# Kernel tuning notes

Hardware: AMD Instinct MI355X
Metric: run time of the kernel (lower is better)

## Reference

```python
import jax, jax.numpy as jnp
import numpy as np

B, T, W, D = 4, 1000, 32, 200
ED, N, DCONV, DTR = 400, 16, 4, 13  # d_inner=2*d_model, d_state, d_conv, dt_rank=ceil(200/16)


def _causal_conv(x, w, b):
    # x: (B, L, ED), depthwise causal conv, kernel DCONV
    L = x.shape[1]
    xp = jnp.pad(x, ((0, 0), (DCONV - 1, 0), (0, 0)))
    y = sum(xp[:, k:k + L, :] * w[:, k] for k in range(DCONV))
    return y + b


def _ssm(x, A_log, Dp, xproj, dtw, dtb):
    # selective scan; x: (B, L, ED)
    A = -jnp.exp(A_log)                      # (ED, N)
    dbc = x @ xproj                          # (B, L, DTR+2N)
    delta, Bm, Cm = dbc[..., :DTR], dbc[..., DTR:DTR + N], dbc[..., DTR + N:]
    dt = jax.nn.softplus(delta @ dtw + dtb)  # (B, L, ED)
    dA = jnp.exp(dt[..., None] * A)                         # (B, L, ED, N)
    dBx = dt[..., None] * Bm[:, :, None, :] * x[..., None]  # (B, L, ED, N)

    def step(h, t):
        dA_t, dBx_t, C_t = t
        h = dA_t * h + dBx_t
        y = jnp.einsum('ben,bn->be', h, C_t)
        return h, y

    h0 = jnp.zeros((x.shape[0], ED, N), x.dtype)
    xs = (dA.transpose(1, 0, 2, 3), dBx.transpose(1, 0, 2, 3), Cm.transpose(1, 0, 2))
    _, ys = jax.lax.scan(step, h0, xs)
    return ys.transpose(1, 0, 2) + Dp * x


def _branch(x, in_proj, conv_w, conv_b, xproj, dtw, dtb, A_log, Dp):
    xz = x @ in_proj
    xp, z = xz[..., :ED], xz[..., ED:]
    xp = jax.nn.silu(_causal_conv(xp, conv_w, conv_b))
    y = _ssm(xp, A_log, Dp, xproj, dtw, dtb)
    return y * jax.nn.silu(z)


def setup_inputs() -> dict:
    key = jax.random.key(0)
    ks = jax.random.split(key, 24)
    s = 0.02
    nrm = lambda k, shape: jax.random.normal(k, shape, jnp.float32) * s
    inp = {}
    inp['input_ids'] = jax.random.normal(ks[0], (B, T, W, D), jnp.float32)
    inp['n_tweets'] = jax.random.randint(ks[1], (B,), 1, T + 1)
    inp['n_words'] = jax.random.randint(ks[2], (B, T), 1, W + 1)
    inp['cls_token'] = jnp.zeros((1, 1, D), jnp.float32)
    inp['w_attn'] = nrm(ks[3], (D, 1))
    inp['b_attn'] = jnp.zeros((1,), jnp.float32)
    inp['norm_w'] = jnp.ones((D,), jnp.float32)
    for i, d in enumerate(('f', 'b')):
        o = i * 8
        inp[f'in_proj_{d}'] = nrm(ks[4 + o], (D, 2 * ED))
        inp[f'conv_w_{d}'] = nrm(ks[5 + o], (ED, DCONV))
        inp[f'conv_b_{d}'] = jnp.zeros((ED,), jnp.float32)
        inp[f'xproj_{d}'] = nrm(ks[6 + o], (ED, DTR + 2 * N))
        inp[f'dtw_{d}'] = nrm(ks[7 + o], (DTR, ED))
        inp[f'dtb_{d}'] = jnp.zeros((ED,), jnp.float32)
        inp[f'A_log_{d}'] = jnp.log(jnp.broadcast_to(jnp.arange(1, N + 1, dtype=jnp.float32), (ED, N)))
        inp[f'D_{d}'] = jnp.ones((ED,), jnp.float32)
    inp['out_proj'] = nrm(ks[20], (ED, D))
    inp['head_w'] = nrm(ks[21], (D, 1))
    inp['head_b'] = jnp.zeros((1,), jnp.float32)
    return inp


def reference(input_ids, n_tweets, n_words, cls_token, w_attn, b_attn, norm_w,
              in_proj_f, conv_w_f, conv_b_f, xproj_f, dtw_f, dtb_f, A_log_f, D_f,
              in_proj_b, conv_w_b, conv_b_b, xproj_b, dtw_b, dtb_b, A_log_b, D_b,
              out_proj, head_w, head_b):
    Bz, Tz, Wz, Dz = input_ids.shape
    # ragged per-tweet attention pooling, fully vectorized with masks
    scores = jnp.squeeze(input_ids @ w_attn, -1) + b_attn[0]        # (B, T, W)
    wmask = jnp.arange(Wz) < n_words[..., None]                     # (B, T, W)
    scores = jnp.where(wmask, scores, -jnp.inf)
    attn = jax.nn.softmax(scores, axis=-1)
    tw = jnp.einsum('btw,btwd->btd', attn, input_ids)               # (B, T, D)
    tmask = jnp.arange(Tz) < n_tweets[:, None]
    tw = jnp.where(tmask[..., None], tw, 0.0)                       # padded tweets stay zero
    pos = Tz // 2
    x = jnp.concatenate([tw[:, :pos], jnp.broadcast_to(cls_token, (Bz, 1, Dz)), tw[:, pos:]], axis=1)
    # one bidirectional Mamba layer: pre-RMSNorm residual block
    xn = x * jax.lax.rsqrt(jnp.mean(x * x, axis=-1, keepdims=True) + 1e-5) * norm_w
    y_f = _branch(xn, in_proj_f, conv_w_f, conv_b_f, xproj_f, dtw_f, dtb_f, A_log_f, D_f)
    y_b = jnp.flip(_branch(jnp.flip(xn, 1), in_proj_b, conv_w_b, conv_b_b, xproj_b, dtw_b, dtb_b, A_log_b, D_b), 1)
    x = x + (y_f + y_b) @ out_proj
    logit = jnp.squeeze(x[:, pos] @ head_w, -1) + head_b[0]
    return jax.nn.sigmoid(logit)
```

## Files before the change

kernel.cpp:

```cpp
#include <hip/hip_runtime.h>
#include <cmath>

#define Bz 4
#define Tz 1000
#define Wz 32
#define Dz 200
#define EDz 400
#define Nz 16
#define DTRz 13
#define Lz 1001
#define POSz 500
#define LPz 501
#define TSTR 512
#define ESP 10
#define NEG_BIG -1e30f

__device__ __forceinline__ float wave_sum(float v) {
#pragma unroll
  for (int o = 32; o; o >>= 1) v += __shfl_xor(v, o);
  return v;
}

__global__ __launch_bounds__(256) void k_front(
    const float* __restrict__ x, const int* __restrict__ n_tweets,
    const int* __restrict__ n_words, const float* __restrict__ w_attn,
    const float* __restrict__ b_attn, const float* __restrict__ norm_w,
    const float* __restrict__ cls, const float* __restrict__ out_proj,
    const float* __restrict__ head_w, const float* __restrict__ ipf,
    const float* __restrict__ ipb, float* __restrict__ xn,
    float* __restrict__ zbuf, float* __restrict__ vbuf) {
  int bid = blockIdx.x;
  int tid = threadIdx.x;
  if (bid < 9) {
    if (bid == 0) {
      __shared__ float hw[Dz];
      if (tid < Dz) hw[tid] = head_w[tid];
      __syncthreads();
      for (int e = tid; e < EDz; e += 256) {
        float acc = 0.f;
        for (int d = 0; d < Dz; d += 4) {
          float4 ov = *(const float4*)(out_proj + e * Dz + d);
          acc += ov.x * hw[d] + ov.y * hw[d + 1] + ov.z * hw[d + 2] + ov.w * hw[d + 3];
        }
        vbuf[e] = acc;
      }
      return;
    }
    int id = bid - 1;
    int br = id >> 2, b = id & 3;
    __shared__ float xs[Dz];
    __shared__ float s_red[4];
    float val = (tid < Dz) ? cls[tid] : 0.f;
    float sq = wave_sum(val * val);
    if ((tid & 63) == 0) s_red[tid >> 6] = sq;
    __syncthreads();
    float tot = s_red[0] + s_red[1] + s_red[2] + s_red[3];
    float scale = rsqrtf(tot * (1.f / Dz) + 1e-5f);
    if (tid < Dz) {
      float o = val * scale * norm_w[tid];
      xs[tid] = o;
      if (br == 0) xn[((size_t)b * Lz + POSz) * Dz + tid] = o;
    }
    __syncthreads();
    const float* ip = br ? ipb : ipf;
    for (int e = tid; e < EDz; e += 256) {
      float acc = 0.f;
      for (int d = 0; d < Dz; ++d) acc += xs[d] * ip[d * (2 * EDz) + EDz + e];
      zbuf[((size_t)br * Bz + b) * EDz + e] = acc;
    }
    return;
  }
  int blk = bid - 9;
  int b = blk / Tz, t = blk - b * Tz;
  int l = (t < POSz) ? t : t + 1;
  float* outp = xn + ((size_t)b * Lz + l) * Dz;
  int ntw = n_tweets[b]; if (ntw > Tz) ntw = Tz;
  if (t >= ntw) { if (tid < Dz) outp[tid] = 0.f; return; }
  int nw = n_words[b * Tz + t]; if (nw > Wz) nw = Wz; if (nw < 1) nw = 1;
  const float* xs = x + ((size_t)(b * Tz + t)) * (Wz * Dz);
  __shared__ float s_attn[Wz];
  __shared__ float s_red[4];
  int w = tid >> 3, j = tid & 7;
  float sc = 0.f;
  if (w < nw) {
    for (int d = j * 4; d < Dz; d += 32) {
      float4 xv = *(const float4*)(xs + w * Dz + d);
      float4 wv = *(const float4*)(w_attn + d);
      sc += xv.x * wv.x + xv.y * wv.y + xv.z * wv.z + xv.w * wv.w;
    }
  }
  sc += __shfl_xor(sc, 1); sc += __shfl_xor(sc, 2); sc += __shfl_xor(sc, 4);
  if (j == 0) s_attn[w] = (w < nw) ? (sc + b_attn[0]) : NEG_BIG;
  __syncthreads();
  if (tid < 64) {
    float s = (tid < Wz) ? s_attn[tid] : NEG_BIG;
    float m = s;
#pragma unroll
    for (int o = 32; o; o >>= 1) m = fmaxf(m, __shfl_xor(m, o));
    float e = (s > 0.5f * NEG_BIG) ? __expf(s - m) : 0.f;
    float tot = wave_sum(e);
    if (tid < Wz) s_attn[tid] = e / tot;
  }
  __syncthreads();
  float val = 0.f;
  if (tid < Dz) {
    for (int ww = 0; ww < nw; ++ww) val += s_attn[ww] * xs[ww * Dz + tid];
  }
  float sq = wave_sum(val * val);
  if ((tid & 63) == 0) s_red[tid >> 6] = sq;
  __syncthreads();
  float tot = s_red[0] + s_red[1] + s_red[2] + s_red[3];
  float scale = rsqrtf(tot * (1.f / Dz) + 1e-5f);
  if (tid < Dz) outp[tid] = val * scale * norm_w[tid];
}

__global__ __launch_bounds__(256) void k_gemm(
    const float* __restrict__ xn, const float* __restrict__ ipf,
    const float* __restrict__ ipb, float* __restrict__ P) {
  int bid = blockIdx.x;
  int brb = bid / 56;
  int rr = bid - brb * 56;
  int tt = rr / 7, ee = rr - tt * 7;
  int br = brb >> 2, b = brb & 3;
  int t0 = tt * 64, e0 = ee * 64;
  const float* ip = br ? ipb : ipf;
  int tid = threadIdx.x;
  int tx = tid & 15, ty = tid >> 4;

  __shared__ float Xs[16][64 + 4];
  __shared__ float Ws[16][64 + 4];

  float acc[4][4];
#pragma unroll
  for (int i = 0; i < 4; ++i)
#pragma unroll
    for (int j = 0; j < 4; ++j) acc[i][j] = 0.f;

  int xr = tid >> 2, xc = (tid & 3) * 4;
  int wr = tid >> 4, wc = (tid & 15) * 4;
  int t = t0 + xr;
  bool tok = (t < LPz);
  int l = br ? (Lz - 1 - t) : t;
  const float* xrow = xn + ((size_t)b * Lz + l) * Dz;

  for (int dk = 0; dk < 200; dk += 16) {
    float xv[4], wv[4];
#pragma unroll
    for (int c = 0; c < 4; ++c) {
      int d = dk + xc + c;
      xv[c] = (tok && d < Dz) ? xrow[d] : 0.f;
    }
    int dw = dk + wr;
#pragma unroll
    for (int c = 0; c < 4; ++c) {
      int e = e0 + wc + c;
      wv[c] = (dw < Dz && e < EDz) ? ip[(size_t)dw * (2 * EDz) + e] : 0.f;
    }
    __syncthreads();
#pragma unroll
    for (int c = 0; c < 4; ++c) Xs[xc + c][xr] = xv[c];
#pragma unroll
    for (int c = 0; c < 4; ++c) Ws[wr][wc + c] = wv[c];
    __syncthreads();
#pragma unroll
    for (int k = 0; k < 16; ++k) {
      float4 a4 = *(const float4*)&Xs[k][ty * 4];
      float4 b4 = *(const float4*)&Ws[k][tx * 4];
      float av[4] = {a4.x, a4.y, a4.z, a4.w};
      float bv[4] = {b4.x, b4.y, b4.z, b4.w};
#pragma unroll
      for (int i = 0; i < 4; ++i)
#pragma unroll
        for (int j = 0; j < 4; ++j) acc[i][j] += av[i] * bv[j];
    }
  }
#pragma unroll
  for (int j = 0; j < 4; ++j) {
    int e = e0 + tx * 4 + j;
    if (e < EDz) {
      float4 o = make_float4(acc[0][j], acc[1][j], acc[2][j], acc[3][j]);
      *(float4*)&P[((size_t)brb * EDz + e) * TSTR + t0 + ty * 4] = o;
    }
  }
}

__global__ __launch_bounds__(256) void k_mid(
    const float* __restrict__ P,
    const float* __restrict__ cwf, const float* __restrict__ cwb,
    const float* __restrict__ cbf, const float* __restrict__ cbb,
    const float* __restrict__ xpjf, const float* __restrict__ xpjb,
    float* __restrict__ xp_t, float* __restrict__ dbcp) {
  int bid = blockIdx.x;
  int esp = bid % ESP;
  int rem = bid / ESP;
  int tc = rem & 7, brb = rem >> 3;
  int br = brb >> 2;
  int tid = threadIdx.x;
  int wave = tid >> 6, lane = tid & 63;
  int t = tc * 64 + lane;
  const float* cw = br ? cwb : cwf;
  const float* cb = br ? cbb : cbf;
  const float* xpj = br ? xpjb : xpjf;

  __shared__ float sred[4][64][45];

  float accq[45];
#pragma unroll
  for (int q = 0; q < 45; ++q) accq[q] = 0.f;

  const float* Pb = P + (size_t)brb * EDz * TSTR;
  int e0 = esp * 40 + wave * 10;
#pragma unroll 2
  for (int i = 0; i < 10; ++i) {
    int e = e0 + i;
    const float* pr = Pb + (size_t)e * TSTR;
    float p0 = (t >= 3) ? pr[t - 3] : 0.f;
    float p1 = (t >= 2) ? pr[t - 2] : 0.f;
    float p2 = (t >= 1) ? pr[t - 1] : 0.f;
    float p3 = pr[t];
    float4 c4 = *(const float4*)(cw + e * 4);
    float a = cb[e] + c4.x * p0 + c4.y * p1 + c4.z * p2 + c4.w * p3;
    float sp = a / (1.f + __expf(-a));
    xp_t[((size_t)brb * EDz + e) * TSTR + t] = sp;
    const float* xq = xpj + e * 45;
#pragma unroll
    for (int q = 0; q < 45; ++q) accq[q] += sp * xq[q];
  }
#pragma unroll
  for (int q = 0; q < 45; ++q) sred[wave][lane][q] = accq[q];
  __syncthreads();
  if (wave < 2) {
#pragma unroll
    for (int q = 0; q < 45; ++q)
      sred[wave][lane][q] += sred[wave + 2][lane][q];
  }
  __syncthreads();
  if (wave == 0) {
    float* dp = dbcp + ((size_t)(esp * 8 + brb) * 45) * TSTR + t;
#pragma unroll
    for (int q = 0; q < 45; ++q)
      dp[(size_t)q * TSTR] = sred[0][lane][q] + sred[1][lane][q];
  }
}

__global__ __launch_bounds__(256) void k_dt2(
    const float* __restrict__ dbcp,
    const float* __restrict__ dtwf, const float* __restrict__ dtwb,
    const float* __restrict__ dtbf, const float* __restrict__ dtbb,
    float* __restrict__ dt_t, float* __restrict__ Bm_t,
    float* __restrict__ Cend) {
  int bid = blockIdx.x;
  int egrp = bid % 11;
  int rem = bid / 11;
  int tc = rem & 7, brb = rem >> 3;
  int br = brb >> 2;
  int tid = threadIdx.x;
  int wave = tid >> 6, lane = tid & 63;
  int t = tc * 64 + lane;
  const size_t espstr = (size_t)8 * 45 * TSTR;

  if (egrp == 10) {
    for (int idx = tid; idx < 16 * 64; idx += 256) {
      int n = idx >> 6, tl = idx & 63;
      size_t base = ((size_t)brb * 45 + 13 + n) * TSTR + tc * 64 + tl;
      float s = 0.f;
#pragma unroll
      for (int esp = 0; esp < ESP; ++esp) s += dbcp[base + esp * espstr];
      Bm_t[((size_t)brb * Nz + n) * TSTR + tc * 64 + tl] = s;
    }
    if (tc == 7 && tid < Nz) {
      size_t base = ((size_t)brb * 45 + 29 + tid) * TSTR + POSz;
      float s = 0.f;
#pragma unroll
      for (int esp = 0; esp < ESP; ++esp) s += dbcp[base + esp * espstr];
      Cend[brb * Nz + tid] = s;
    }
    return;
  }

  __shared__ float dfin[DTRz][64];
  for (int idx = tid; idx < DTRz * 64; idx += 256) {
    int q = idx >> 6, tl = idx & 63;
    size_t base = ((size_t)brb * 45 + q) * TSTR + tc * 64 + tl;
    float s = 0.f;
#pragma unroll
    for (int esp = 0; esp < ESP; ++esp) s += dbcp[base + esp * espstr];
    dfin[q][tl] = s;
  }
  __syncthreads();
  const float* dtw = br ? dtwb : dtwf;
  const float* dtb = br ? dtbb : dtbf;
  float dq[DTRz];
#pragma unroll
  for (int q = 0; q < DTRz; ++q) dq[q] = dfin[q][lane];
  int e0 = egrp * 40 + wave * 10;
#pragma unroll 2
  for (int i = 0; i < 10; ++i) {
    int e = e0 + i;
    float s = dtb[e];
#pragma unroll
    for (int q = 0; q < DTRz; ++q) s += dq[q] * dtw[q * EDz + e];
    float dtv = (s > 20.f) ? s : log1pf(__expf(s));
    dt_t[((size_t)brb * EDz + e) * TSTR + t] = dtv;
  }
}

__global__ __launch_bounds__(64) void k_scan(
    const float* __restrict__ xp_t, const float* __restrict__ dt_t,
    const float* __restrict__ Bm_t, const float* __restrict__ Cend,
    const float* __restrict__ Alogf, const float* __restrict__ Alogb,
    const float* __restrict__ Dpf, const float* __restrict__ Dpb,
    const float* __restrict__ zbuf, const float* __restrict__ vbuf,
    float* __restrict__ ybuf) {
  int blk = blockIdx.x;
  int br = blk / (Bz * EDz);
  int rem = blk - br * (Bz * EDz);
  int b = rem / EDz, e = rem - b * EDz;
  int lane = threadIdx.x;
  const float* A_log = br ? Alogb : Alogf;
  const float* Dp = br ? Dpb : Dpf;
  float A[Nz];
  {
    const float4* ap = (const float4*)(A_log + e * Nz);
#pragma unroll
    for (int q = 0; q < 4; ++q) {
      float4 a4 = ap[q];
      A[q * 4 + 0] = -__expf(a4.x); A[q * 4 + 1] = -__expf(a4.y);
      A[q * 4 + 2] = -__expf(a4.z); A[q * 4 + 3] = -__expf(a4.w);
    }
  }
  size_t base = ((size_t)(br * Bz + b) * EDz + e) * TSTR;
  const float* dtp = dt_t + base;
  const float* xpp = xp_t + base;
  const float* bmp = Bm_t + (size_t)(br * Bz + b) * Nz * TSTR;
  float loc = 0.f;
#pragma unroll
  for (int c = 0; c < 8; ++c) {
    int t = c * 64 + lane;
    if (t < LPz) loc += dtp[t];
  }
  float Stot = wave_sum(loc);
  float acc[Nz];
#pragma unroll
  for (int n = 0; n < Nz; ++n) acc[n] = 0.f;
  float carry = 0.f;
  for (int c = 0; c < 8; ++c) {
    int t = c * 64 + lane;
    bool act = t < LPz;
    float dtt = 0.f, xv = 0.f;
    if (act) { dtt = dtp[t]; xv = xpp[t]; }
    float s = dtt;
#pragma unroll
    for (int o = 1; o < 64; o <<= 1) {
      float u = __shfl_up(s, o);
      s += (lane >= o) ? u : 0.f;
    }
    float S = carry + s;
    carry += __shfl(s, 63);
    float wt = dtt * xv;
    float decay = Stot - S;
#pragma unroll
    for (int n = 0; n < Nz; ++n) {
      float bv = 0.f;
      if (act) bv = bmp[n * TSTR + t];
      acc[n] += __expf(A[n] * decay) * wt * bv;
    }
  }
#pragma unroll
  for (int o = 32; o; o >>= 1) {
#pragma unroll
    for (int n = 0; n < Nz; ++n) acc[n] += __shfl_xor(acc[n], o);
  }
  if (lane == 0) {
    float y = Dp[e] * xpp[LPz - 1];
#pragma unroll
    for (int n = 0; n < Nz; ++n) y += Cend[(br * Bz + b) * Nz + n] * acc[n];
    float zz = zbuf[((size_t)br * Bz + b) * EDz + e];
    float sz = zz / (1.f + __expf(-zz));
    ybuf[((size_t)br * Bz + b) * EDz + e] = y * sz * vbuf[e];
  }
}

__global__ __launch_bounds__(256) void k_final(
    const float* __restrict__ cls, const float* __restrict__ head_w,
    const float* __restrict__ head_b, const float* __restrict__ ybuf,
    float* __restrict__ out) {
  int tid = threadIdx.x;
  int b = tid >> 6, lane = tid & 63;
  float acc = 0.f;
  for (int e = lane; e < EDz; e += 64)
    acc += ybuf[(size_t)b * EDz + e] + ybuf[(size_t)(Bz + b) * EDz + e];
  for (int d = lane; d < Dz; d += 64) acc += cls[d] * head_w[d];
  acc = wave_sum(acc);
  if (lane == 0) out[b] = 1.f / (1.f + __expf(-(acc + head_b[0])));
}

extern "C" void kernel_launch(void* const* d_in, const int* in_sizes, int n_in,
                              void* d_out, int out_size, void* d_ws, size_t ws_size,
                              hipStream_t stream) {
  const float* input_ids = (const float*)d_in[0];
  const int* n_tweets = (const int*)d_in[1];
  const int* n_words = (const int*)d_in[2];
  const float* cls = (const float*)d_in[3];
  const float* w_attn = (const float*)d_in[4];
  const float* b_attn = (const float*)d_in[5];
  const float* norm_w = (const float*)d_in[6];
  const float* ip[2] = {(const float*)d_in[7], (const float*)d_in[15]};
  const float* cw[2] = {(const float*)d_in[8], (const float*)d_in[16]};
  const float* cb[2] = {(const float*)d_in[9], (const float*)d_in[17]};
  const float* xpj[2] = {(const float*)d_in[10], (const float*)d_in[18]};
  const float* dtw[2] = {(const float*)d_in[11], (const float*)d_in[19]};
  const float* dtbp[2] = {(const float*)d_in[12], (const float*)d_in[20]};
  const float* Alog[2] = {(const float*)d_in[13], (const float*)d_in[21]};
  const float* Dpp[2] = {(const float*)d_in[14], (const float*)d_in[22]};
  const float* out_proj = (const float*)d_in[23];
  const float* head_w = (const float*)d_in[24];
  const float* head_b = (const float*)d_in[25];
  float* out = (float*)d_out;

  float* ws = (float*)d_ws;
  float* xn = ws;
  float* Pbuf = xn + 800800;
  float* xp_t = Pbuf + 1638400;
  float* dt_t = xp_t + 1638400;
  float* Bm_t = dt_t + 1638400;
  float* dbcp = Bm_t + 65536;
  float* Cend = dbcp + 1843200;
  float* zbuf = Cend + 128;
  float* vbuf = zbuf + 3200;
  float* ybuf = vbuf + 400;

  hipLaunchKernelGGL(k_front, dim3(9 + Bz * Tz), dim3(256), 0, stream,
                     input_ids, n_tweets, n_words, w_attn, b_attn, norm_w,
                     cls, out_proj, head_w, ip[0], ip[1], xn, zbuf, vbuf);
  hipLaunchKernelGGL(k_gemm, dim3(2 * Bz * 8 * 7), dim3(256), 0, stream,
                     xn, ip[0], ip[1], Pbuf);
  hipLaunchKernelGGL(k_mid, dim3(2 * Bz * 8 * ESP), dim3(256), 0, stream,
                     Pbuf, cw[0], cw[1], cb[0], cb[1], xpj[0], xpj[1],
                     xp_t, dbcp);
  hipLaunchKernelGGL(k_dt2, dim3(2 * Bz * 8 * 11), dim3(256), 0, stream,
                     dbcp, dtw[0], dtw[1], dtbp[0], dtbp[1],
                     dt_t, Bm_t, Cend);
  hipLaunchKernelGGL(k_scan, dim3(2 * Bz * EDz), dim3(64), 0, stream,
                     xp_t, dt_t, Bm_t, Cend, Alog[0], Alog[1], Dpp[0], Dpp[1],
                     zbuf, vbuf, ybuf);
  hipLaunchKernelGGL(k_final, dim3(1), dim3(256), 0, stream,
                     cls, head_w, head_b, ybuf, out);
}
```

Measured before the change: 106.9 us.

## Fuse all stages into one persistent cooperative kernel with grid syncs

Merges the six separate kernels (front pooling, GEMM, conv/xproj, dt, scan, final) into one cooperative persistent kernel. Blocks loop over tasks in each phase, and grid.sync separates the phases. The aim is to remove the launch gaps and tail effects between kernels. The costs are the grid-wide barriers, a grid capped at 1024 blocks, and the scan phase changing from 64-thread blocks to one wave per task. The register pressure of the fused code may also lower occupancy.

```diff
diff --git a/kernel.cpp b/kernel.cpp
--- a/kernel.cpp
+++ b/kernel.cpp
@@ -1,5 +1,8 @@
 #include <hip/hip_runtime.h>
+#include <hip/hip_cooperative_groups.h>
 #include <cmath>
+
+namespace cg = cooperative_groups;
 
 #define Bz 4
 #define Tz 1000
@@ -21,429 +24,438 @@
   return v;
 }
 
-__global__ __launch_bounds__(256) void k_front(
+union SMem {
+  struct { float attn[Wz]; float red[4]; float xs[Dz]; } f;
+  struct { float Xs[16][68]; float Ws[16][68]; } g;
+  struct { float sred[64][46]; } m;
+  struct { float dfin[DTRz][64]; } d;
+};
+
+__global__ __launch_bounds__(256) void k_all(
     const float* __restrict__ x, const int* __restrict__ n_tweets,
     const int* __restrict__ n_words, const float* __restrict__ w_attn,
     const float* __restrict__ b_attn, const float* __restrict__ norm_w,
     const float* __restrict__ cls, const float* __restrict__ out_proj,
-    const float* __restrict__ head_w, const float* __restrict__ ipf,
-    const float* __restrict__ ipb, float* __restrict__ xn,
-    float* __restrict__ zbuf, float* __restrict__ vbuf) {
-  int bid = blockIdx.x;
-  int tid = threadIdx.x;
-  if (bid < 9) {
-    if (bid == 0) {
-      __shared__ float hw[Dz];
-      if (tid < Dz) hw[tid] = head_w[tid];
-      __syncthreads();
+    const float* __restrict__ head_w, const float* __restrict__ head_b,
+    const float* __restrict__ ipf, const float* __restrict__ ipb,
+    const float* __restrict__ cwf, const float* __restrict__ cwb,
+    const float* __restrict__ cbf, const float* __restrict__ cbb,
+    const float* __restrict__ xpjf, const float* __restrict__ xpjb,
+    const float* __restrict__ dtwf, const float* __restrict__ dtwb,
+    const float* __restrict__ dtbf, const float* __restrict__ dtbb,
+    const float* __restrict__ Alogf, const float* __restrict__ Alogb,
+    const float* __restrict__ Dpf, const float* __restrict__ Dpb,
+    float* __restrict__ xn, float* __restrict__ Pbuf,
+    float* __restrict__ xp_t, float* __restrict__ dt_t,
+    float* __restrict__ Bm_t, float* __restrict__ dbcp,
+    float* __restrict__ Cend, float* __restrict__ zbuf,
+    float* __restrict__ vbuf, float* __restrict__ ybuf,
+    float* __restrict__ outp) {
+  cg::grid_group grid = cg::this_grid();
+  __shared__ SMem sh;
+  const int bid = blockIdx.x;
+  const int G = gridDim.x;
+  const int tid = threadIdx.x;
+  const int wave = tid >> 6, lane = tid & 63;
+
+  for (int task = bid; task < 9 + Bz * Tz; task += G) {
+    if (task == 0) {
       for (int e = tid; e < EDz; e += 256) {
         float acc = 0.f;
         for (int d = 0; d < Dz; d += 4) {
           float4 ov = *(const float4*)(out_proj + e * Dz + d);
-          acc += ov.x * hw[d] + ov.y * hw[d + 1] + ov.z * hw[d + 2] + ov.w * hw[d + 3];
+          acc += ov.x * head_w[d] + ov.y * head_w[d + 1] +
+                 ov.z * head_w[d + 2] + ov.w * head_w[d + 3];
         }
         vbuf[e] = acc;
       }
-      return;
-    }
-    int id = bid - 1;
-    int br = id >> 2, b = id & 3;
-    __shared__ float xs[Dz];
-    __shared__ float s_red[4];
-    float val = (tid < Dz) ? cls[tid] : 0.f;
-    float sq = wave_sum(val * val);
-    if ((tid & 63) == 0) s_red[tid >> 6] = sq;
-    __syncthreads();
-    float tot = s_red[0] + s_red[1] + s_red[2] + s_red[3];
-    float scale = rsqrtf(tot * (1.f / Dz) + 1e-5f);
-    if (tid < Dz) {
-      float o = val * scale * norm_w[tid];
-      xs[tid] = o;
-      if (br == 0) xn[((size_t)b * Lz + POSz) * Dz + tid] = o;
-    }
-    __syncthreads();
+    } else if (task < 9) {
+      int id = task - 1;
+      int br = id >> 2, b = id & 3;
+      float val = (tid < Dz) ? cls[tid] : 0.f;
+      float sq = wave_sum(val * val);
+      if (lane == 0) sh.f.red[wave] = sq;
+      __syncthreads();
+      float tot = sh.f.red[0] + sh.f.red[1] + sh.f.red[2] + sh.f.red[3];
+      float scale = rsqrtf(tot * (1.f / Dz) + 1e-5f);
+      if (tid < Dz) {
+        float o = val * scale * norm_w[tid];
+        sh.f.xs[tid] = o;
+        if (br == 0) xn[((size_t)b * Lz + POSz) * Dz + tid] = o;
+      }
+      __syncthreads();
+      const float* ip = br ? ipb : ipf;
+      for (int e = tid; e < EDz; e += 256) {
+        float acc = 0.f;
+        for (int d = 0; d < Dz; ++d) acc += sh.f.xs[d] * ip[d * (2 * EDz) + EDz + e];
+        zbuf[((size_t)br * Bz + b) * EDz + e] = acc;
+      }
+    } else {
+      int pt = task - 9;
+      int b = pt / Tz, t = pt - b * Tz;
+      int l = (t < POSz) ? t : t + 1;
+      float* outr = xn + ((size_t)b * Lz + l) * Dz;
+      int ntw = n_tweets[b]; if (ntw > Tz) ntw = Tz;
+      if (t >= ntw) {
+        if (tid < Dz) outr[tid] = 0.f;
+      } else {
+        int nw = n_words[b * Tz + t]; if (nw > Wz) nw = Wz; if (nw < 1) nw = 1;
+        const float* xs = x + ((size_t)(b * Tz + t)) * (Wz * Dz);
+        int w = tid >> 3, j = tid & 7;
+        float sc = 0.f;
+        if (w < nw) {
+          for (int d = j * 4; d < Dz; d += 32) {
+            float4 xv = *(const float4*)(xs + w * Dz + d);
+            float4 wv = *(const float4*)(w_attn + d);
+            sc += xv.x * wv.x + xv.y * wv.y + xv.z * wv.z + xv.w * wv.w;
+          }
+        }
+        sc += __shfl_xor(sc, 1); sc += __shfl_xor(sc, 2); sc += __shfl_xor(sc, 4);
+        if (j == 0) sh.f.attn[w] = (w < nw) ? (sc + b_attn[0]) : NEG_BIG;
+        __syncthreads();
+        if (tid < 64) {
+          float s = (tid < Wz) ? sh.f.attn[tid] : NEG_BIG;
+          float m = s;
+#pragma unroll
+          for (int o = 32; o; o >>= 1) m = fmaxf(m, __shfl_xor(m, o));
+          float e = (s > 0.5f * NEG_BIG) ? __expf(s - m) : 0.f;
+          float tot = wave_sum(e);
+          if (tid < Wz) sh.f.attn[tid] = e / tot;
+        }
+        __syncthreads();
+        float val = 0.f;
+        if (tid < Dz) {
+          for (int ww = 0; ww < nw; ++ww) val += sh.f.attn[ww] * xs[ww * Dz + tid];
+        }
+        float sq = wave_sum(val * val);
+        if (lane == 0) sh.f.red[wave] = sq;
+        __syncthreads();
+        float tot = sh.f.red[0] + sh.f.red[1] + sh.f.red[2] + sh.f.red[3];
+        float scale = rsqrtf(tot * (1.f / Dz) + 1e-5f);
+        if (tid < Dz) outr[tid] = val * scale * norm_w[tid];
+      }
+    }
+    __syncthreads();
+  }
+  __threadfence();
+  grid.sync();
+
+  for (int task = bid; task < 8 * 56; task += G) {
+    int brb = task / 56;
+    int rr = task - brb * 56;
+    int tt = rr / 7, ee = rr - tt * 7;
+    int br = brb >> 2, b = brb & 3;
+    int t0 = tt * 64, e0 = ee * 64;
     const float* ip = br ? ipb : ipf;
-    for (int e = tid; e < EDz; e += 256) {
-      float acc = 0.f;
-      for (int d = 0; d < Dz; ++d) acc += xs[d] * ip[d * (2 * EDz) + EDz + e];
-      zbuf[((size_t)br * Bz + b) * EDz + e] = acc;
-    }
-    return;
-  }
-  int blk = bid - 9;
-  int b = blk / Tz, t = blk - b * Tz;
-  int l = (t < POSz) ? t : t + 1;
-  float* outp = xn + ((size_t)b * Lz + l) * Dz;
-  int ntw = n_tweets[b]; if (ntw > Tz) ntw = Tz;
-  if (t >= ntw) { if (tid < Dz) outp[tid] = 0.f; return; }
-  int nw = n_words[b * Tz + t]; if (nw > Wz) nw = Wz; if (nw < 1) nw = 1;
-  const float* xs = x + ((size_t)(b * Tz + t)) * (Wz * Dz);
-  __shared__ float s_attn[Wz];
-  __shared__ float s_red[4];
-  int w = tid >> 3, j = tid & 7;
-  float sc = 0.f;
-  if (w < nw) {
-    for (int d = j * 4; d < Dz; d += 32) {
-      float4 xv = *(const float4*)(xs + w * Dz + d);
-      float4 wv = *(const float4*)(w_attn + d);
-      sc += xv.x * wv.x + xv.y * wv.y + xv.z * wv.z + xv.w * wv.w;
-    }
-  }
-  sc += __shfl_xor(sc, 1); sc += __shfl_xor(sc, 2); sc += __shfl_xor(sc, 4);
-  if (j == 0) s_attn[w] = (w < nw) ? (sc + b_attn[0]) : NEG_BIG;
-  __syncthreads();
-  if (tid < 64) {
-    float s = (tid < Wz) ? s_attn[tid] : NEG_BIG;
-    float m = s;
-#pragma unroll
-    for (int o = 32; o; o >>= 1) m = fmaxf(m, __shfl_xor(m, o));
-    float e = (s > 0.5f * NEG_BIG) ? __expf(s - m) : 0.f;
-    float tot = wave_sum(e);
-    if (tid < Wz) s_attn[tid] = e / tot;
-  }
-  __syncthreads();
-  float val = 0.f;
-  if (tid < Dz) {
-    for (int ww = 0; ww < nw; ++ww) val += s_attn[ww] * xs[ww * Dz + tid];
-  }
-  float sq = wave_sum(val * val);
-  if ((tid & 63) == 0) s_red[tid >> 6] = sq;
-  __syncthreads();
-  float tot = s_red[0] + s_red[1] + s_red[2] + s_red[3];
-  float scale = rsqrtf(tot * (1.f / Dz) + 1e-5f);
-  if (tid < Dz) outp[tid] = val * scale * norm_w[tid];
-}
-
-__global__ __launch_bounds__(256) void k_gemm(
-    const float* __restrict__ xn, const float* __restrict__ ipf,
-    const float* __restrict__ ipb, float* __restrict__ P) {
-  int bid = blockIdx.x;
-  int brb = bid / 56;
-  int rr = bid - brb * 56;
-  int tt = rr / 7, ee = rr - tt * 7;
-  int br = brb >> 2, b = brb & 3;
-  int t0 = tt * 64, e0 = ee * 64;
-  const float* ip = br ? ipb : ipf;
-  int tid = threadIdx.x;
-  int tx = tid & 15, ty = tid >> 4;
-
-  __shared__ float Xs[16][64 + 4];
-  __shared__ float Ws[16][64 + 4];
-
-  float acc[4][4];
-#pragma unroll
-  for (int i = 0; i < 4; ++i)
-#pragma unroll
-    for (int j = 0; j < 4; ++j) acc[i][j] = 0.f;
-
-  int xr = tid >> 2, xc = (tid & 3) * 4;
-  int wr = tid >> 4, wc = (tid & 15) * 4;
-  int t = t0 + xr;
-  bool tok = (t < LPz);
-  int l = br ? (Lz - 1 - t) : t;
-  const float* xrow = xn + ((size_t)b * Lz + l) * Dz;
-
-  for (int dk = 0; dk < 200; dk += 16) {
-    float xv[4], wv[4];
-#pragma unroll
-    for (int c = 0; c < 4; ++c) {
-      int d = dk + xc + c;
-      xv[c] = (tok && d < Dz) ? xrow[d] : 0.f;
-    }
-    int dw = dk + wr;
-#pragma unroll
-    for (int c = 0; c < 4; ++c) {
-      int e = e0 + wc + c;
-      wv[c] = (dw < Dz && e < EDz) ? ip[(size_t)dw * (2 * EDz) + e] : 0.f;
-    }
-    __syncthreads();
-#pragma unroll
-    for (int c = 0; c < 4; ++c) Xs[xc + c][xr] = xv[c];
-#pragma unroll
-    for (int c = 0; c < 4; ++c) Ws[wr][wc + c] = wv[c];
-    __syncthreads();
-#pragma unroll
-    for (int k = 0; k < 16; ++k) {
-      float4 a4 = *(const float4*)&Xs[k][ty * 4];
-      float4 b4 = *(const float4*)&Ws[k][tx * 4];
-      float av[4] = {a4.x, a4.y, a4.z, a4.w};
-      float bv[4] = {b4.x, b4.y, b4.z, b4.w};
-#pragma unroll
-      for (int i = 0; i < 4; ++i)
-#pragma unroll
-        for (int j = 0; j < 4; ++j) acc[i][j] += av[i] * bv[j];
-    }
-  }
-#pragma unroll
-  for (int j = 0; j < 4; ++j) {
-    int e = e0 + tx * 4 + j;
-    if (e < EDz) {
-      float4 o = make_float4(acc[0][j], acc[1][j], acc[2][j], acc[3][j]);
-      *(float4*)&P[((size_t)brb * EDz + e) * TSTR + t0 + ty * 4] = o;
-    }
-  }
-}
-
-__global__ __launch_bounds__(256) void k_mid(
-    const float* __restrict__ P,
-    const float* __restrict__ cwf, const float* __restrict__ cwb,
-    const float* __restrict__ cbf, const float* __restrict__ cbb,
-    const float* __restrict__ xpjf, const float* __restrict__ xpjb,
-    float* __restrict__ xp_t, float* __restrict__ dbcp) {
-  int bid = blockIdx.x;
-  int esp = bid % ESP;
-  int rem = bid / ESP;
-  int tc = rem & 7, brb = rem >> 3;
-  int br = brb >> 2;
-  int tid = threadIdx.x;
-  int wave = tid >> 6, lane = tid & 63;
-  int t = tc * 64 + lane;
-  const float* cw = br ? cwb : cwf;
-  const float* cb = br ? cbb : cbf;
-  const float* xpj = br ? xpjb : xpjf;
-
-  __shared__ float sred[4][64][45];
-
-  float accq[45];
-#pragma unroll
-  for (int q = 0; q < 45; ++q) accq[q] = 0.f;
-
-  const float* Pb = P + (size_t)brb * EDz * TSTR;
-  int e0 = esp * 40 + wave * 10;
+    int tx = tid & 15, ty = tid >> 4;
+    float acc[4][4];
+#pragma unroll
+    for (int i = 0; i < 4; ++i)
+#pragma unroll
+      for (int j = 0; j < 4; ++j) acc[i][j] = 0.f;
+    int xr = tid >> 2, xc = (tid & 3) * 4;
+    int wr = tid >> 4, wc = (tid & 15) * 4;
+    int t = t0 + xr;
+    bool tok = (t < LPz);
+    int l = br ? (Lz - 1 - t) : t;
+    const float* xrow = xn + ((size_t)b * Lz + l) * Dz;
+    for (int dk = 0; dk < 200; dk += 16) {
+      float xv[4], wv[4];
+#pragma unroll
+      for (int c = 0; c < 4; ++c) {
+        int d = dk + xc + c;
+        xv[c] = (tok && d < Dz) ? xrow[d] : 0.f;
+      }
+      int dw = dk + wr;
+#pragma unroll
+      for (int c = 0; c < 4; ++c) {
+        int e = e0 + wc + c;
+        wv[c] = (dw < Dz && e < EDz) ? ip[(size_t)dw * (2 * EDz) + e] : 0.f;
+      }
+      __syncthreads();
+#pragma unroll
+      for (int c = 0; c < 4; ++c) sh.g.Xs[xc + c][xr] = xv[c];
+#pragma unroll
+      for (int c = 0; c < 4; ++c) sh.g.Ws[wr][wc + c] = wv[c];
+      __syncthreads();
+#pragma unroll
+      for (int k = 0; k < 16; ++k) {
+        float4 a4 = *(const float4*)&sh.g.Xs[k][ty * 4];
+        float4 b4 = *(const float4*)&sh.g.Ws[k][tx * 4];
+        float av[4] = {a4.x, a4.y, a4.z, a4.w};
+        float bv[4] = {b4.x, b4.y, b4.z, b4.w};
+#pragma unroll
+        for (int i = 0; i < 4; ++i)
+#pragma unroll
+          for (int j = 0; j < 4; ++j) acc[i][j] += av[i] * bv[j];
+      }
+    }
+#pragma unroll
+    for (int j = 0; j < 4; ++j) {
+      int e = e0 + tx * 4 + j;
+      if (e < EDz) {
+        float4 o = make_float4(acc[0][j], acc[1][j], acc[2][j], acc[3][j]);
+        *(float4*)&Pbuf[((size_t)brb * EDz + e) * TSTR + t0 + ty * 4] = o;
+      }
+    }
+    __syncthreads();
+  }
+  __threadfence();
+  grid.sync();
+
+  for (int task = bid; task < 8 * 8 * ESP; task += G) {
+    int esp = task % ESP;
+    int rem = task / ESP;
+    int tc = rem & 7, brb = rem >> 3;
+    int br = brb >> 2;
+    int t = tc * 64 + lane;
+    const float* cw = br ? cwb : cwf;
+    const float* cb = br ? cbb : cbf;
+    const float* xpj = br ? xpjb : xpjf;
+    float accq[45];
+#pragma unroll
+    for (int q = 0; q < 45; ++q) accq[q] = 0.f;
+    const float* Pb = Pbuf + (size_t)brb * EDz * TSTR;
+    int e0 = esp * 40 + wave * 10;
 #pragma unroll 2
-  for (int i = 0; i < 10; ++i) {
-    int e = e0 + i;
-    const float* pr = Pb + (size_t)e * TSTR;
-    float p0 = (t >= 3) ? pr[t - 3] : 0.f;
-    float p1 = (t >= 2) ? pr[t - 2] : 0.f;
-    float p2 = (t >= 1) ? pr[t - 1] : 0.f;
-    float p3 = pr[t];
-    float4 c4 = *(const float4*)(cw + e * 4);
-    float a = cb[e] + c4.x * p0 + c4.y * p1 + c4.z * p2 + c4.w * p3;
-    float sp = a / (1.f + __expf(-a));
-    xp_t[((size_t)brb * EDz + e) * TSTR + t] = sp;
-    const float* xq = xpj + e * 45;
-#pragma unroll
-    for (int q = 0; q < 45; ++q) accq[q] += sp * xq[q];
-  }
-#pragma unroll
-  for (int q = 0; q < 45; ++q) sred[wave][lane][q] = accq[q];
-  __syncthreads();
-  if (wave < 2) {
-#pragma unroll
-    for (int q = 0; q < 45; ++q)
-      sred[wave][lane][q] += sred[wave + 2][lane][q];
-  }
-  __syncthreads();
-  if (wave == 0) {
-    float* dp = dbcp + ((size_t)(esp * 8 + brb) * 45) * TSTR + t;
-#pragma unroll
-    for (int q = 0; q < 45; ++q)
-      dp[(size_t)q * TSTR] = sred[0][lane][q] + sred[1][lane][q];
-  }
-}
-
-__global__ __launch_bounds__(256) void k_dt2(
-    const float* __restrict__ dbcp,
-    const float* __restrict__ dtwf, const float* __restrict__ dtwb,
-    const float* __restrict__ dtbf, const float* __restrict__ dtbb,
-    float* __restrict__ dt_t, float* __restrict__ Bm_t,
-    float* __restrict__ Cend) {
-  int bid = blockIdx.x;
-  int egrp = bid % 11;
-  int rem = bid / 11;
-  int tc = rem & 7, brb = rem >> 3;
-  int br = brb >> 2;
-  int tid = threadIdx.x;
-  int wave = tid >> 6, lane = tid & 63;
-  int t = tc * 64 + lane;
-  const size_t espstr = (size_t)8 * 45 * TSTR;
-
-  if (egrp == 10) {
-    for (int idx = tid; idx < 16 * 64; idx += 256) {
-      int n = idx >> 6, tl = idx & 63;
-      size_t base = ((size_t)brb * 45 + 13 + n) * TSTR + tc * 64 + tl;
-      float s = 0.f;
-#pragma unroll
-      for (int esp = 0; esp < ESP; ++esp) s += dbcp[base + esp * espstr];
-      Bm_t[((size_t)brb * Nz + n) * TSTR + tc * 64 + tl] = s;
-    }
-    if (tc == 7 && tid < Nz) {
-      size_t base = ((size_t)brb * 45 + 29 + tid) * TSTR + POSz;
-      float s = 0.f;
-#pragma unroll
-      for (int esp = 0; esp < ESP; ++esp) s += dbcp[base + esp * espstr];
-      Cend[brb * Nz + tid] = s;
-    }
-    return;
-  }
-
-  __shared__ float dfin[DTRz][64];
-  for (int idx = tid; idx < DTRz * 64; idx += 256) {
-    int q = idx >> 6, tl = idx & 63;
-    size_t base = ((size_t)brb * 45 + q) * TSTR + tc * 64 + tl;
-    float s = 0.f;
-#pragma unroll
-    for (int esp = 0; esp < ESP; ++esp) s += dbcp[base + esp * espstr];
-    dfin[q][tl] = s;
-  }
-  __syncthreads();
-  const float* dtw = br ? dtwb : dtwf;
-  const float* dtb = br ? dtbb : dtbf;
-  float dq[DTRz];
-#pragma unroll
-  for (int q = 0; q < DTRz; ++q) dq[q] = dfin[q][lane];
-  int e0 = egrp * 40 + wave * 10;
+    for (int i = 0; i < 10; ++i) {
+      int e = e0 + i;
+      const float* pr = Pb + (size_t)e * TSTR;
+      float p0 = (t >= 3) ? pr[t - 3] : 0.f;
+      float p1 = (t >= 2) ? pr[t - 2] : 0.f;
+      float p2 = (t >= 1) ? pr[t - 1] : 0.f;
+      float p3 = pr[t];
+      float4 c4 = *(const float4*)(cw + e * 4);
+      float a = cb[e] + c4.x * p0 + c4.y * p1 + c4.z * p2 + c4.w * p3;
+      float sp = a / (1.f + __expf(-a));
+      xp_t[((size_t)brb * EDz + e) * TSTR + t] = sp;
+      const float* xq = xpj + e * 45;
+#pragma unroll
+      for (int q = 0; q < 45; ++q) accq[q] += sp * xq[q];
+    }
+    if (wave == 0) {
+#pragma unroll
+      for (int q = 0; q < 45; ++q) sh.m.sred[lane][q] = accq[q];
+    }
+    __syncthreads();
+    if (wave == 1) {
+#pragma unroll
+      for (int q = 0; q < 45; ++q) sh.m.sred[lane][q] += accq[q];
+    }
+    __syncthreads();
+    if (wave == 2) {
+#pragma unroll
+      for (int q = 0; q < 45; ++q) sh.m.sred[lane][q] += accq[q];
+    }
+    __syncthreads();
+    if (wave == 3) {
+#pragma unroll
+      for (int q = 0; q < 45; ++q) sh.m.sred[lane][q] += accq[q];
+    }
+    __syncthreads();
+    if (wave == 0) {
+      float* dp = dbcp + ((size_t)(esp * 8 + brb) * 45) * TSTR + t;
+#pragma unroll
+      for (int q = 0; q < 45; ++q) dp[(size_t)q * TSTR] = sh.m.sred[lane][q];
+    }
+    __syncthreads();
+  }
+  __threadfence();
+  grid.sync();
+
+  for (int task = bid; task < 8 * 8 * 11; task += G) {
+    int egrp = task % 11;
+    int rem = task / 11;
+    int tc = rem & 7, brb = rem >> 3;
+    int br = brb >> 2;
+    int t = tc * 64 + lane;
+    const size_t espstr = (size_t)8 * 45 * TSTR;
+    if (egrp == 10) {
+      for (int idx = tid; idx < 16 * 64; idx += 256) {
+        int n = idx >> 6, tl = idx & 63;
+        size_t base = ((size_t)brb * 45 + 13 + n) * TSTR + tc * 64 + tl;
+        float s = 0.f;
+#pragma unroll
+        for (int esp = 0; esp < ESP; ++esp) s += dbcp[base + esp * espstr];
+        Bm_t[((size_t)brb * Nz + n) * TSTR + tc * 64 + tl] = s;
+      }
+      if (tc == 7 && tid < Nz) {
+        size_t base = ((size_t)brb * 45 + 29 + tid) * TSTR + POSz;
+        float s = 0.f;
+#pragma unroll
+        for (int esp = 0; esp < ESP; ++esp) s += dbcp[base + esp * espstr];
+        Cend[brb * Nz + tid] = s;
+      }
+    } else {
+      for (int idx = tid; idx < DTRz * 64; idx += 256) {
+        int q = idx >> 6, tl = idx & 63;
+        size_t base = ((size_t)brb * 45 + q) * TSTR + tc * 64 + tl;
+        float s = 0.f;
+#pragma unroll
+        for (int esp = 0; esp < ESP; ++esp) s += dbcp[base + esp * espstr];
+        sh.d.dfin[q][tl] = s;
+      }
+      __syncthreads();
+      const float* dtw = br ? dtwb : dtwf;
+      const float* dtb = br ? dtbb : dtbf;
+      float dq[DTRz];
+#pragma unroll
+      for (int q = 0; q < DTRz; ++q) dq[q] = sh.d.dfin[q][lane];
+      int e0 = egrp * 40 + wave * 10;
 #pragma unroll 2
-  for (int i = 0; i < 10; ++i) {
-    int e = e0 + i;
-    float s = dtb[e];
-#pragma unroll
-    for (int q = 0; q < DTRz; ++q) s += dq[q] * dtw[q * EDz + e];
-    float dtv = (s > 20.f) ? s : log1pf(__expf(s));
-    dt_t[((size_t)brb * EDz + e) * TSTR + t] = dtv;
-  }
-}
-
-__global__ __launch_bounds__(64) void k_scan(
-    const float* __restrict__ xp_t, const float* __restrict__ dt_t,
-    const float* __restrict__ Bm_t, const float* __restrict__ Cend,
-    const float* __restrict__ Alogf, const float* __restrict__ Alogb,
-    const float* __restrict__ Dpf, const float* __restrict__ Dpb,
-    const float* __restrict__ zbuf, const float* __restrict__ vbuf,
-    float* __restrict__ ybuf) {
-  int blk = blockIdx.x;
-  int br = blk / (Bz * EDz);
-  int rem = blk - br * (Bz * EDz);
-  int b = rem / EDz, e = rem - b * EDz;
-  int lane = threadIdx.x;
-  const float* A_log = br ? Alogb : Alogf;
-  const float* Dp = br ? Dpb : Dpf;
-  float A[Nz];
-  {
-    const float4* ap = (const float4*)(A_log + e * Nz);
-#pragma unroll
-    for (int q = 0; q < 4; ++q) {
-      float4 a4 = ap[q];
-      A[q * 4 + 0] = -__expf(a4.x); A[q * 4 + 1] = -__expf(a4.y);
-      A[q * 4 + 2] = -__expf(a4.z); A[q * 4 + 3] = -__expf(a4.w);
-    }
-  }
-  size_t base = ((size_t)(br * Bz + b) * EDz + e) * TSTR;
-  const float* dtp = dt_t + base;
-  const float* xpp = xp_t + base;
-  const float* bmp = Bm_t + (size_t)(br * Bz + b) * Nz * TSTR;
-  float loc = 0.f;
-#pragma unroll
-  for (int c = 0; c < 8; ++c) {
-    int t = c * 64 + lane;
-    if (t < LPz) loc += dtp[t];
-  }
-  float Stot = wave_sum(loc);
-  float acc[Nz];
-#pragma unroll
-  for (int n = 0; n < Nz; ++n) acc[n] = 0.f;
-  float carry = 0.f;
-  for (int c = 0; c < 8; ++c) {
-    int t = c * 64 + lane;
-    bool act = t < LPz;
-    float dtt = 0.f, xv = 0.f;
-    if (act) { dtt = dtp[t]; xv = xpp[t]; }
-    float s = dtt;
-#pragma unroll
-    for (int o = 1; o < 64; o <<= 1) {
-      float u = __shfl_up(s, o);
-      s += (lane >= o) ? u : 0.f;
-    }
-    float S = carry + s;
-    carry += __shfl(s, 63);
-    float wt = dtt * xv;
-    float decay = Stot - S;
-#pragma unroll
-    for (int n = 0; n < Nz; ++n) {
-      float bv = 0.f;
-      if (act) bv = bmp[n * TSTR + t];
-      acc[n] += __expf(A[n] * decay) * wt * bv;
-    }
-  }
-#pragma unroll
-  for (int o = 32; o; o >>= 1) {
-#pragma unroll
-    for (int n = 0; n < Nz; ++n) acc[n] += __shfl_xor(acc[n], o);
-  }
-  if (lane == 0) {
-    float y = Dp[e] * xpp[LPz - 1];
-#pragma unroll
-    for (int n = 0; n < Nz; ++n) y += Cend[(br * Bz + b) * Nz + n] * acc[n];
-    float zz = zbuf[((size_t)br * Bz + b) * EDz + e];
-    float sz = zz / (1.f + __expf(-zz));
-    ybuf[((size_t)br * Bz + b) * EDz + e] = y * sz * vbuf[e];
-  }
-}
-
-__global__ __launch_bounds__(256) void k_final(
-    const float* __restrict__ cls, const float* __restrict__ head_w,
-    const float* __restrict__ head_b, const float* __restrict__ ybuf,
-    float* __restrict__ out) {
-  int tid = threadIdx.x;
-  int b = tid >> 6, lane = tid & 63;
-  float acc = 0.f;
-  for (int e = lane; e < EDz; e += 64)
-    acc += ybuf[(size_t)b * EDz + e] + ybuf[(size_t)(Bz + b) * EDz + e];
-  for (int d = lane; d < Dz; d += 64) acc += cls[d] * head_w[d];
-  acc = wave_sum(acc);
-  if (lane == 0) out[b] = 1.f / (1.f + __expf(-(acc + head_b[0])));
+      for (int i = 0; i < 10; ++i) {
+        int e = e0 + i;
+        float s = dtb[e];
+#pragma unroll
+        for (int q = 0; q < DTRz; ++q) s += dq[q] * dtw[q * EDz + e];
+        float dtv = (s > 20.f) ? s : log1pf(__expf(s));
+        dt_t[((size_t)brb * EDz + e) * TSTR + t] = dtv;
+      }
+    }
+    __syncthreads();
+  }
+  __threadfence();
+  grid.sync();
+
+  for (int task = bid * 4 + wave; task < 2 * Bz * EDz; task += G * 4) {
+    int br = task / (Bz * EDz);
+    int rem = task - br * (Bz * EDz);
+    int b = rem / EDz, e = rem - b * EDz;
+    const float* A_log = br ? Alogb : Alogf;
+    const float* Dp = br ? Dpb : Dpf;
+    float A[Nz];
+    {
+      const float4* ap = (const float4*)(A_log + e * Nz);
+#pragma unroll
+      for (int q = 0; q < 4; ++q) {
+        float4 a4 = ap[q];
+        A[q * 4 + 0] = -__expf(a4.x); A[q * 4 + 1] = -__expf(a4.y);
+        A[q * 4 + 2] = -__expf(a4.z); A[q * 4 + 3] = -__expf(a4.w);
+      }
+    }
+    size_t base = ((size_t)(br * Bz + b) * EDz + e) * TSTR;
+    const float* dtp = dt_t + base;
+    const float* xpp = xp_t + base;
+    const float* bmp = Bm_t + (size_t)(br * Bz + b) * Nz * TSTR;
+    float loc = 0.f;
+#pragma unroll
+    for (int c = 0; c < 8; ++c) {
+      int t = c * 64 + lane;
+      if (t < LPz) loc += dtp[t];
+    }
+    float Stot = wave_sum(loc);
+    float acc[Nz];
+#pragma unroll
+    for (int n = 0; n < Nz; ++n) acc[n] = 0.f;
+    float carry = 0.f;
+    for (int c = 0; c < 8; ++c) {
+      int t = c * 64 + lane;
+      bool act = t < LPz;
+      float dtt = 0.f, xv = 0.f;
+      if (act) { dtt = dtp[t]; xv = xpp[t]; }
+      float s = dtt;
+#pragma unroll
+      for (int o = 1; o < 64; o <<= 1) {
+        float u = __shfl_up(s, o);
+        s += (lane >= o) ? u : 0.f;
+      }
+      float S = carry + s;
+      carry += __shfl(s, 63);
+      float wt = dtt * xv;
+      float decay = Stot - S;
+#pragma unroll
+      for (int n = 0; n < Nz; ++n) {
+        float bv = 0.f;
+        if (act) bv = bmp[n * TSTR + t];
+        acc[n] += __expf(A[n] * decay) * wt * bv;
+      }
+    }
+#pragma unroll
+    for (int o = 32; o; o >>= 1) {
+#pragma unroll
+      for (int n = 0; n < Nz; ++n) acc[n] += __shfl_xor(acc[n], o);
+    }
+    if (lane == 0) {
+      float y = Dp[e] * xpp[LPz - 1];
+#pragma unroll
+      for (int n = 0; n < Nz; ++n) y += Cend[(br * Bz + b) * Nz + n] * acc[n];
+      float zz = zbuf[((size_t)br * Bz + b) * EDz + e];
+      float sz = zz / (1.f + __expf(-zz));
+      ybuf[((size_t)br * Bz + b) * EDz + e] = y * sz * vbuf[e];
+    }
+  }
+  __threadfence();
+  grid.sync();
+
+  if (bid == 0) {
+    int b = tid >> 6;
+    float acc = 0.f;
+    for (int e = lane; e < EDz; e += 64)
+      acc += ybuf[(size_t)b * EDz + e] + ybuf[(size_t)(Bz + b) * EDz + e];
+    for (int d = lane; d < Dz; d += 64) acc += cls[d] * head_w[d];
+    acc = wave_sum(acc);
+    if (lane == 0) outp[b] = 1.f / (1.f + __expf(-(acc + head_b[0])));
+  }
 }
 
 extern "C" void kernel_launch(void* const* d_in, const int* in_sizes, int n_in,
                               void* d_out, int out_size, void* d_ws, size_t ws_size,
                               hipStream_t stream) {
-  const float* input_ids = (const float*)d_in[0];
-  const int* n_tweets = (const int*)d_in[1];
-  const int* n_words = (const int*)d_in[2];
-  const float* cls = (const float*)d_in[3];
-  const float* w_attn = (const float*)d_in[4];
-  const float* b_attn = (const float*)d_in[5];
-  const float* norm_w = (const float*)d_in[6];
-  const float* ip[2] = {(const float*)d_in[7], (const float*)d_in[15]};
-  const float* cw[2] = {(const float*)d_in[8], (const float*)d_in[16]};
-  const float* cb[2] = {(const float*)d_in[9], (const float*)d_in[17]};
-  const float* xpj[2] = {(const float*)d_in[10], (const float*)d_in[18]};
-  const float* dtw[2] = {(const float*)d_in[11], (const float*)d_in[19]};
-  const float* dtbp[2] = {(const float*)d_in[12], (const float*)d_in[20]};
-  const float* Alog[2] = {(const float*)d_in[13], (const float*)d_in[21]};
-  const float* Dpp[2] = {(const float*)d_in[14], (const float*)d_in[22]};
-  const float* out_proj = (const float*)d_in[23];
-  const float* head_w = (const float*)d_in[24];
-  const float* head_b = (const float*)d_in[25];
-  float* out = (float*)d_out;
+  const float* x_ = (const float*)d_in[0];
+  const int* ntw_ = (const int*)d_in[1];
+  const int* nwd_ = (const int*)d_in[2];
+  const float* cls_ = (const float*)d_in[3];
+  const float* wat_ = (const float*)d_in[4];
+  const float* bat_ = (const float*)d_in[5];
+  const float* nw_ = (const float*)d_in[6];
+  const float* ipf_ = (const float*)d_in[7];
+  const float* cwf_ = (const float*)d_in[8];
+  const float* cbf_ = (const float*)d_in[9];
+  const float* xpjf_ = (const float*)d_in[10];
+  const float* dtwf_ = (const float*)d_in[11];
+  const float* dtbf_ = (const float*)d_in[12];
+  const float* Alf_ = (const float*)d_in[13];
+  const float* Dpf_ = (const float*)d_in[14];
+  const float* ipb_ = (const float*)d_in[15];
+  const float* cwb_ = (const float*)d_in[16];
+  const float* cbb_ = (const float*)d_in[17];
+  const float* xpjb_ = (const float*)d_in[18];
+  const float* dtwb_ = (const float*)d_in[19];
+  const float* dtbb_ = (const float*)d_in[20];
+  const float* Alb_ = (const float*)d_in[21];
+  const float* Dpb_ = (const float*)d_in[22];
+  const float* opj_ = (const float*)d_in[23];
+  const float* hw_ = (const float*)d_in[24];
+  const float* hb_ = (const float*)d_in[25];
+  float* out_ = (float*)d_out;
 
   float* ws = (float*)d_ws;
-  float* xn = ws;
-  float* Pbuf = xn + 800800;
-  float* xp_t = Pbuf + 1638400;
-  float* dt_t = xp_t + 1638400;
-  float* Bm_t = dt_t + 1638400;
-  float* dbcp = Bm_t + 65536;
-  float* Cend = dbcp + 1843200;
-  float* zbuf = Cend + 128;
-  float* vbuf = zbuf + 3200;
-  float* ybuf = vbuf + 400;
-
-  hipLaunchKernelGGL(k_front, dim3(9 + Bz * Tz), dim3(256), 0, stream,
-                     input_ids, n_tweets, n_words, w_attn, b_attn, norm_w,
-                     cls, out_proj, head_w, ip[0], ip[1], xn, zbuf, vbuf);
-  hipLaunchKernelGGL(k_gemm, dim3(2 * Bz * 8 * 7), dim3(256), 0, stream,
-                     xn, ip[0], ip[1], Pbuf);
-  hipLaunchKernelGGL(k_mid, dim3(2 * Bz * 8 * ESP), dim3(256), 0, stream,
-                     Pbuf, cw[0], cw[1], cb[0], cb[1], xpj[0], xpj[1],
-                     xp_t, dbcp);
-  hipLaunchKernelGGL(k_dt2, dim3(2 * Bz * 8 * 11), dim3(256), 0, stream,
-                     dbcp, dtw[0], dtw[1], dtbp[0], dtbp[1],
-                     dt_t, Bm_t, Cend);
-  hipLaunchKernelGGL(k_scan, dim3(2 * Bz * EDz), dim3(64), 0, stream,
-                     xp_t, dt_t, Bm_t, Cend, Alog[0], Alog[1], Dpp[0], Dpp[1],
-                     zbuf, vbuf, ybuf);
-  hipLaunchKernelGGL(k_final, dim3(1), dim3(256), 0, stream,
-                     cls, head_w, head_b, ybuf, out);
+  float* xn_ = ws;
+  float* Pbuf_ = xn_ + 800800;
+  float* xpt_ = Pbuf_ + 1638400;
+  float* dtt_ = xpt_ + 1638400;
+  float* Bmt_ = dtt_ + 1638400;
+  float* dbcp_ = Bmt_ + 65536;
+  float* Cend_ = dbcp_ + 1843200;
+  float* zbuf_ = Cend_ + 128;
+  float* vbuf_ = zbuf_ + 3200;
+  float* ybuf_ = vbuf_ + 400;
+
+  int occ = 0;
+  hipOccupancyMaxActiveBlocksPerMultiprocessor(&occ, k_all, 256, 0);
+  if (occ < 1) occ = 1;
+  int G = occ * 256;
+  if (G > 1024) G = 1024;
+
+  void* args[] = {
+    (void*)&x_, (void*)&ntw_, (void*)&nwd_, (void*)&wat_, (void*)&bat_,
+    (void*)&nw_, (void*)&cls_, (void*)&opj_, (void*)&hw_, (void*)&hb_,
+    (void*)&ipf_, (void*)&ipb_, (void*)&cwf_, (void*)&cwb_, (void*)&cbf_,
+    (void*)&cbb_, (void*)&xpjf_, (void*)&xpjb_, (void*)&dtwf_, (void*)&dtwb_,
+    (void*)&dtbf_, (void*)&dtbb_, (void*)&Alf_, (void*)&Alb_, (void*)&Dpf_,
+    (void*)&Dpb_, (void*)&xn_, (void*)&Pbuf_, (void*)&xpt_, (void*)&dtt_,
+    (void*)&Bmt_, (void*)&dbcp_, (void*)&Cend_, (void*)&zbuf_, (void*)&vbuf_,
+    (void*)&ybuf_, (void*)&out_
+  };
+  hipLaunchCooperativeKernel(k_all, dim3(G), dim3(256), args, 0, stream);
 }
```

Result: slower. 417.3 us (+290.3%).

## Map one wavefront per tweet in attention pooling, removing block syncs

Applied to the files above, without the earlier changes.

The attention-pooling part of the front kernel now gives each 64-lane wavefront one tweet, so each 256-thread block handles four tweets and the grid shrinks by four. Scores, softmax, weighted sum and RMSNorm all use wave shuffles instead of shared memory and __syncthreads, and the weighted sum loads and stores with float4. The aim is to cut block-level synchronisation and per-block overhead in a memory-bound phase. In exchange, each weighted-sum pass uses only 50 of 64 lanes, and the score loop has two lanes each reading 100 contiguous floats.

```diff
diff --git a/kernel.cpp b/kernel.cpp
--- a/kernel.cpp
+++ b/kernel.cpp
@@ -31,6 +31,7 @@
     float* __restrict__ zbuf, float* __restrict__ vbuf) {
   int bid = blockIdx.x;
   int tid = threadIdx.x;
+  int wave = tid >> 6, lane = tid & 63;
   if (bid < 9) {
     if (bid == 0) {
       __shared__ float hw[Dz];
@@ -70,48 +71,57 @@
     }
     return;
   }
-  int blk = bid - 9;
-  int b = blk / Tz, t = blk - b * Tz;
+  int bt = (bid - 9) * 4 + wave;
+  int b = bt / Tz, t = bt - b * Tz;
   int l = (t < POSz) ? t : t + 1;
-  float* outp = xn + ((size_t)b * Lz + l) * Dz;
+  float* outr = xn + ((size_t)b * Lz + l) * Dz;
   int ntw = n_tweets[b]; if (ntw > Tz) ntw = Tz;
-  if (t >= ntw) { if (tid < Dz) outp[tid] = 0.f; return; }
+  if (t >= ntw) {
+    if (lane < 50) *(float4*)(outr + lane * 4) = make_float4(0.f, 0.f, 0.f, 0.f);
+    return;
+  }
   int nw = n_words[b * Tz + t]; if (nw > Wz) nw = Wz; if (nw < 1) nw = 1;
   const float* xs = x + ((size_t)(b * Tz + t)) * (Wz * Dz);
-  __shared__ float s_attn[Wz];
-  __shared__ float s_red[4];
-  int w = tid >> 3, j = tid & 7;
+  int h = lane & 1, w = lane >> 1;
   float sc = 0.f;
   if (w < nw) {
-    for (int d = j * 4; d < Dz; d += 32) {
-      float4 xv = *(const float4*)(xs + w * Dz + d);
-      float4 wv = *(const float4*)(w_attn + d);
+    const float* xr = xs + w * Dz + h * 100;
+    const float* wr = w_attn + h * 100;
+#pragma unroll
+    for (int i = 0; i < 25; ++i) {
+      float4 xv = *(const float4*)(xr + i * 4);
+      float4 wv = *(const float4*)(wr + i * 4);
       sc += xv.x * wv.x + xv.y * wv.y + xv.z * wv.z + xv.w * wv.w;
     }
   }
-  sc += __shfl_xor(sc, 1); sc += __shfl_xor(sc, 2); sc += __shfl_xor(sc, 4);
-  if (j == 0) s_attn[w] = (w < nw) ? (sc + b_attn[0]) : NEG_BIG;
-  __syncthreads();
-  if (tid < 64) {
-    float s = (tid < Wz) ? s_attn[tid] : NEG_BIG;
-    float m = s;
-#pragma unroll
-    for (int o = 32; o; o >>= 1) m = fmaxf(m, __shfl_xor(m, o));
-    float e = (s > 0.5f * NEG_BIG) ? __expf(s - m) : 0.f;
-    float tot = wave_sum(e);
-    if (tid < Wz) s_attn[tid] = e / tot;
-  }
-  __syncthreads();
-  float val = 0.f;
-  if (tid < Dz) {
-    for (int ww = 0; ww < nw; ++ww) val += s_attn[ww] * xs[ww * Dz + tid];
-  }
-  float sq = wave_sum(val * val);
-  if ((tid & 63) == 0) s_red[tid >> 6] = sq;
-  __syncthreads();
-  float tot = s_red[0] + s_red[1] + s_red[2] + s_red[3];
-  float scale = rsqrtf(tot * (1.f / Dz) + 1e-5f);
-  if (tid < Dz) outp[tid] = val * scale * norm_w[tid];
+  sc += __shfl_xor(sc, 1);
+  float scv = (w < nw) ? (sc + b_attn[0]) : NEG_BIG;
+  float m = scv;
+#pragma unroll
+  for (int o = 32; o; o >>= 1) m = fmaxf(m, __shfl_xor(m, o));
+  float en = __expf(scv - m);
+  float es = (h == 0) ? en : 0.f;
+  float tot = wave_sum(es);
+  en /= tot;
+  float4 val = make_float4(0.f, 0.f, 0.f, 0.f);
+  const float* xc = xs + lane * 4;
+  for (int ww = 0; ww < nw; ++ww) {
+    float aw = __shfl(en, 2 * ww);
+    if (lane < 50) {
+      float4 xv = *(const float4*)(xc + ww * Dz);
+      val.x += aw * xv.x; val.y += aw * xv.y;
+      val.z += aw * xv.z; val.w += aw * xv.w;
+    }
+  }
+  float sq = (lane < 50) ? (val.x * val.x + val.y * val.y + val.z * val.z + val.w * val.w) : 0.f;
+  sq = wave_sum(sq);
+  float scale = rsqrtf(sq * (1.f / Dz) + 1e-5f);
+  if (lane < 50) {
+    float4 nw4 = *(const float4*)(norm_w + lane * 4);
+    float4 o = make_float4(val.x * scale * nw4.x, val.y * scale * nw4.y,
+                           val.z * scale * nw4.z, val.w * scale * nw4.w);
+    *(float4*)(outr + lane * 4) = o;
+  }
 }
 
 __global__ __launch_bounds__(256) void k_gemm(
@@ -430,7 +440,7 @@
   float* vbuf = zbuf + 3200;
   float* ybuf = vbuf + 400;
 
-  hipLaunchKernelGGL(k_front, dim3(9 + Bz * Tz), dim3(256), 0, stream,
+  hipLaunchKernelGGL(k_front, dim3(9 + Bz * Tz / 4), dim3(256), 0, stream,
                      input_ids, n_tweets, n_words, w_attn, b_attn, norm_w,
                      cls, out_proj, head_w, ip[0], ip[1], xn, zbuf, vbuf);
   hipLaunchKernelGGL(k_gemm, dim3(2 * Bz * 8 * 7), dim3(256), 0, stream,
```

Result: no change. 107.4 us (+0.5%).
